# Kernel tuning notes

Hardware: AMD Instinct MI355X
Metric: run time of the kernel (lower is better)

The kernel has to match this reference:

```python
import jax, jax.numpy as jnp
import numpy as np

EPS = 1e-5

def setup_inputs() -> dict:
    key = jax.random.key(0)
    ks = jax.random.split(key, 8)
    B, C, O, H, W = 4, 256, 256, 64, 64
    x = jax.random.normal(ks[0], (B, C, H, W), jnp.float32)
    # offset/mask conv: 27 = deformable_groups(1) * 3 * kh * kw; small init so sampling points stay near grid
    w_off = jax.random.normal(ks[1], (27, C, 3, 3), jnp.float32) * 0.01
    b_off = jnp.zeros((27,), jnp.float32)
    weight = jax.random.normal(ks[2], (O, C, 3, 3), jnp.float32) * (1.0 / np.sqrt(C * 9))
    bias = jnp.zeros((O,), jnp.float32)
    gamma = 1.0 + 0.1 * jax.random.normal(ks[3], (O,), jnp.float32)
    beta = 0.1 * jax.random.normal(ks[4], (O,), jnp.float32)
    run_mean = 0.05 * jax.random.normal(ks[5], (O,), jnp.float32)
    run_var = jax.random.uniform(ks[6], (O,), jnp.float32, 0.5, 1.5)
    return {"x": x, "w_off": w_off, "b_off": b_off, "weight": weight, "bias": bias,
            "gamma": gamma, "beta": beta, "run_mean": run_mean, "run_var": run_var}

def reference(x, w_off, b_off, weight, bias, gamma, beta, run_mean, run_var):
    B, C, H, W = x.shape
    O = weight.shape[0]
    K = 9  # 3x3 kernel taps
    # conv_offset_mask: standard 3x3 conv, pad 1 -> (B, 27, H, W)
    om = jax.lax.conv_general_dilated(
        x, w_off, window_strides=(1, 1), padding=[(1, 1), (1, 1)],
        dimension_numbers=("NCHW", "OIHW", "NCHW")) + b_off[None, :, None, None]
    dy, dx = om[:, :K], om[:, K:2 * K]            # (B,9,H,W) learned offsets
    mask = jax.nn.sigmoid(om[:, 2 * K:])           # (B,9,H,W) modulation
    # base sampling grid for 3x3, stride 1, pad 1, dilation 1
    ky, kx = jnp.meshgrid(jnp.arange(3), jnp.arange(3), indexing="ij")
    ky = ky.reshape(K, 1, 1).astype(x.dtype)
    kx = kx.reshape(K, 1, 1).astype(x.dtype)
    base_y = (jnp.arange(H, dtype=x.dtype) - 1.0)[None, :, None] + ky  # (9,H,1)
    base_x = (jnp.arange(W, dtype=x.dtype) - 1.0)[None, None, :] + kx  # (9,1,W)
    py = dy + base_y  # (B,9,H,W) absolute sample coords
    px = dx + base_x
    y0 = jnp.floor(py); x0 = jnp.floor(px)
    ly = py - y0; lx = px - x0
    y0i = y0.astype(jnp.int32); x0i = x0.astype(jnp.int32)
    xf = x.reshape(B, C, H * W)

    def corner(yi, xi, wgt):
        valid = (yi >= 0) & (yi < H) & (xi >= 0) & (xi < W)  # zero-pad outside
        yc = jnp.clip(yi, 0, H - 1)
        xc = jnp.clip(xi, 0, W - 1)
        idx = (yc * W + xc).reshape(B, 1, -1)                # (B,1,9HW)
        g = jnp.take_along_axis(xf, idx, axis=2)             # (B,C,9HW)
        return g * (wgt * valid.astype(x.dtype)).reshape(B, 1, -1)

    val = (corner(y0i, x0i, (1 - ly) * (1 - lx))
           + corner(y0i, x0i + 1, (1 - ly) * lx)
           + corner(y0i + 1, x0i, ly * (1 - lx))
           + corner(y0i + 1, x0i + 1, ly * lx))
    val = val.reshape(B, C, K, H, W) * mask[:, None]          # modulated im2col
    out = jnp.einsum("bckhw,ock->bohw", val, weight.reshape(O, C, K))
    out = out + bias[None, :, None, None]
    # BN (eval mode, running stats) + ReLU
    inv = jax.lax.rsqrt(run_var + EPS)
    out = gamma[None, :, None, None] * (out - run_mean[None, :, None, None]) * inv[None, :, None, None] + beta[None, :, None, None]
    return jax.nn.relu(out)
```

## Files before the change

### kernel.cpp

```cpp
#include <hip/hip_runtime.h>
#include <math.h>

#define HW_ 4096
#define N_ 16384
#define RS2 1168
#define LDS_PK 37376
#define LDS_W4 38528
#define LDS_TOT 43136

typedef _Float16 f16x4 __attribute__((ext_vector_type(4)));
typedef _Float16 f16x8 __attribute__((ext_vector_type(8)));
typedef float f32x4 __attribute__((ext_vector_type(4)));
typedef unsigned short u16x8 __attribute__((ext_vector_type(8)));


static __device__ __forceinline__ unsigned short f2h(float f) {
  _Float16 h = (_Float16)f;
  return __builtin_bit_cast(unsigned short, h);
}
static __device__ __forceinline__ f32x4 madv(f32x4 a, float s, f32x4 c) {
  c.x = fmaf(a.x, s, c.x);
  c.y = fmaf(a.y, s, c.y);
  c.z = fmaf(a.z, s, c.z);
  c.w = fmaf(a.w, s, c.w);
  return c;
}

__global__ __launch_bounds__(256) void transp_kernel(const float* __restrict__ x,
                                                     float* __restrict__ xT) {
  __shared__ float t[64][65];
  int bid = blockIdx.x;
  int b = bid >> 8, cg = (bid >> 6) & 3, h = bid & 63;
  int tid = threadIdx.x;
  int l16 = tid & 15, r16 = tid >> 4;
  const float* xs = x + (size_t)(b * 256 + cg * 64) * HW_ + h * 64;
#pragma unroll
  for (int j = 0; j < 4; ++j) {
    int c = j * 16 + r16;
    f32x4 v = *(const f32x4*)(xs + (size_t)c * HW_ + l16 * 4);
    t[c][l16 * 4 + 0] = v.x;
    t[c][l16 * 4 + 1] = v.y;
    t[c][l16 * 4 + 2] = v.z;
    t[c][l16 * 4 + 3] = v.w;
  }
  __syncthreads();
  float* xd = xT + (size_t)(b * HW_ + h * 64) * 256 + cg * 64;
#pragma unroll
  for (int j = 0; j < 4; ++j) {
    int w2 = j * 16 + r16;
    f32x4 v;
#pragma unroll
    for (int i = 0; i < 4; ++i) v[i] = t[l16 * 4 + i][w2];
    *(f32x4*)(xd + (size_t)w2 * 256 + l16 * 4) = v;
  }
}

__global__ __launch_bounds__(256) void wprep_kernel(
    const float* __restrict__ weight, const float* __restrict__ w_off,
    const float* __restrict__ bias, const float* __restrict__ gamma,
    const float* __restrict__ beta, const float* __restrict__ rmean,
    const float* __restrict__ rvar, unsigned short* __restrict__ Wt,
    unsigned short* __restrict__ Woff, float* __restrict__ scale,
    float* __restrict__ shift) {
  int o = blockIdx.x, tid = threadIdx.x;
  __shared__ unsigned short wl[2304];
  __shared__ unsigned short wol[2304];
  const float* wrow = weight + (size_t)o * 2304;
  const float* worow = w_off + (size_t)o * 2304;
  bool do_off = (o < 32);
#pragma unroll
  for (int j = 0; j < 9; ++j) {
    int flat = tid + j * 256;
    int c = flat / 9, k = flat - 9 * c;
    int cb = c >> 6, cloc = c & 31;
    int ks = (k << 1) | ((c >> 5) & 1);
    int dst = (cb * 18 + ks) * 32 + cloc;
    wl[dst] = f2h(wrow[flat]);
    if (do_off) wol[dst] = f2h((o < 27) ? worow[flat] : 0.f);
  }
  __syncthreads();
  for (int it = tid; it < 288; it += 256) {
    int chunk = it >> 2, part = it & 3;
    *(u16x8*)&Wt[((size_t)chunk * 256 + o) * 32 + part * 8] =
        *(const u16x8*)&wl[chunk * 32 + part * 8];
    if (do_off)
      *(u16x8*)&Woff[((size_t)chunk * 32 + o) * 32 + part * 8] =
          *(const u16x8*)&wol[chunk * 32 + part * 8];
  }
  if (o == 0) {
    float inv = rsqrtf(rvar[tid] + 1e-5f);
    float sc = gamma[tid] * inv;
    scale[tid] = sc;
    shift[tid] = beta[tid] + sc * (bias[tid] - rmean[tid]);
  }
}

__global__ __launch_bounds__(512) void fused_kernel(
    const float* __restrict__ xT, const unsigned short* __restrict__ Wt,
    const unsigned short* __restrict__ Woff, const float* __restrict__ b_off,
    const float* __restrict__ scale, const float* __restrict__ shift,
    float* __restrict__ out) {
  __shared__ __align__(16) char smem[LDS_TOT];
  float* om_lds = (float*)smem;
  unsigned int* pk_lds = (unsigned int*)(smem + LDS_PK);
  float* w4_lds = (float*)(smem + LDS_W4);

  int bid = blockIdx.x;
  int swz = (bid & 7) * 64 + (bid >> 3);
  int nbase = swz * 32;
  int b = nbase >> 12;
  int h = (nbase >> 6) & 63;
  int wb = nbase & 32;

  int tid = threadIdx.x;
  int lane = tid & 63;
  int wv = tid >> 6;
  int m15 = lane & 15, q = lane >> 4;
  int sn = tid >> 4;
  int cs = tid & 15;

  const char* xb = (const char*)xT + (size_t)b * (HW_ * 256 * 4);
  char* ldr = smem + sn * RS2 + ((cs >> 3) << 6) + (cs & 7) * 8;

  int mf = (wv >> 1) & 1, nf1 = wv & 1;
  f32x4 aoff = (f32x4){0.f, 0.f, 0.f, 0.f};
  for (int cb = 0; cb < 4; ++cb) {
    {
      const char* xc = xb + cb * 256 + cs * 16;
#pragma unroll
      for (int k = 0; k < 9; ++k) {
        int ky = k / 3, kx = k - 3 * (k / 3);
        int yy = h + ky - 1, xx = wb + sn + kx - 1;
        f32x4 v = (f32x4){0.f, 0.f, 0.f, 0.f};
        if (((unsigned)yy < 64u) && ((unsigned)xx < 64u))
          v = *(const f32x4*)(xc + (size_t)(yy * 64 + xx) * 1024);
        *(f16x4*)(ldr + k * 128) = __builtin_convertvector(v, f16x4);
      }
    }
    __syncthreads();
    if (wv < 4) {
#pragma unroll
      for (int ks = 0; ks < 18; ++ks) {
        f16x8 a = *(const f16x8*)(Woff + ((cb * 18 + ks) * 32 + mf * 16 + m15) * 32 + q * 8);
        f16x8 bb = *(const f16x8*)(smem + (nf1 * 16 + m15) * RS2 + ks * 64 + q * 16);
        aoff = __builtin_amdgcn_mfma_f32_16x16x32_f16(a, bb, aoff, 0, 0, 0);
      }
    }
    __syncthreads();
  }
  if (wv < 4) {
#pragma unroll
    for (int r = 0; r < 4; ++r)
      om_lds[(mf * 16 + q * 4 + r) * 32 + nf1 * 16 + m15] = aoff[r];
  }
  __syncthreads();

  if (tid < 288) {
    int k = tid >> 5, pxl = tid & 31;
    float dy = om_lds[k * 32 + pxl] + b_off[k];
    float dx = om_lds[(k + 9) * 32 + pxl] + b_off[k + 9];
    float z = om_lds[(k + 18) * 32 + pxl] + b_off[k + 18];
    float ms = 1.f / (1.f + expf(-z));
    int ky = k / 3, kx = k - 3 * ky;
    float py = dy + (float)(h - 1 + ky);
    float pxf = dx + (float)(wb + pxl - 1 + kx);
    float fy0 = floorf(py), fx0 = floorf(pxf);
    float ly = py - fy0, lx = pxf - fx0;
    int iy0 = (int)fy0, ix0 = (int)fx0;
    bool vy0 = (iy0 >= 0) && (iy0 < 64);
    bool vy1 = (iy0 >= -1) && (iy0 < 63);
    bool vx0 = (ix0 >= 0) && (ix0 < 64);
    bool vx1 = (ix0 >= -1) && (ix0 < 63);
    int yA = min(max(iy0, 0), 63), yB = min(max(iy0 + 1, 0), 63);
    int xA = min(max(ix0, 0), 63), xB = min(max(ix0 + 1, 0), 63);
    pk_lds[k * 32 + pxl] = (unsigned)(yA * 64 + xA) | ((unsigned)(xB - xA) << 12) |
                           ((unsigned)(yB - yA) << 13);
    float* wp = w4_lds + (k * 32 + pxl) * 4;
    wp[0] = (1.f - ly) * (1.f - lx) * ms * ((vy0 && vx0) ? 1.f : 0.f);
    wp[1] = (1.f - ly) * lx * ms * ((vy0 && vx1) ? 1.f : 0.f);
    wp[2] = ly * (1.f - lx) * ms * ((vy1 && vx0) ? 1.f : 0.f);
    wp[3] = ly * lx * ms * ((vy1 && vx1) ? 1.f : 0.f);
  }
  __syncthreads();

  f32x4 acc[2][2];
#pragma unroll
  for (int mfi = 0; mfi < 2; ++mfi)
#pragma unroll
    for (int nf = 0; nf < 2; ++nf) acc[mfi][nf] = (f32x4){0.f, 0.f, 0.f, 0.f};

  f16x4 sv[9];
#define GATHER(CB)                                                     \
  {                                                                    \
    const char* xc = xb + (CB) * 256 + cs * 16;                        \
    _Pragma("unroll") for (int k = 0; k < 9; ++k) {                    \
      unsigned pv = pk_lds[k * 32 + sn];                               \
      f32x4 w4v = *(const f32x4*)(w4_lds + (k * 32 + sn) * 4);         \
      const char* p00 = xc + ((size_t)(pv & 0xFFFu) << 10);            \
      int dxb = (int)(pv & 0x1000u) >> 2;             \
      int dyb = (int)(pv & 0x2000u) << 3;             \
      f32x4 c00 = *(const f32x4*)(p00);                                \
      f32x4 c01 = *(const f32x4*)(p00 + dxb);                          \
      f32x4 c10 = *(const f32x4*)(p00 + dyb);                          \
      f32x4 c11 = *(const f32x4*)(p00 + dyb + dxb);                    \
      f32x4 v = (f32x4){0.f, 0.f, 0.f, 0.f};                           \
      v = madv(c00, w4v.x, v);                                         \
      v = madv(c01, w4v.y, v);                                         \
      v = madv(c10, w4v.z, v);                                         \
      v = madv(c11, w4v.w, v);                                         \
      sv[k] = __builtin_convertvector(v, f16x4);                       \
    }                                                                  \
  }

  GATHER(0);
  for (int cb = 0; cb < 4; ++cb) {
    {
#pragma unroll
      for (int k = 0; k < 9; ++k) *(f16x4*)(ldr + k * 128) = sv[k];
    }
    __syncthreads();
    if (cb < 3) GATHER(cb + 1);
    {
      const unsigned short* wtk = Wt + (size_t)(cb * 18) * 8192 + (wv * 32 + m15) * 32 + q * 8;
#pragma unroll
      for (int ks = 0; ks < 18; ++ks) {
        const unsigned short* wp2 = wtk + ks * 8192;
        f16x8 a0 = *(const f16x8*)(wp2);
        f16x8 a1 = *(const f16x8*)(wp2 + 512);
#pragma unroll
        for (int nf = 0; nf < 2; ++nf) {
          f16x8 bb = *(const f16x8*)(smem + (nf * 16 + m15) * RS2 + ks * 64 + q * 16);
          acc[0][nf] = __builtin_amdgcn_mfma_f32_16x16x32_f16(a0, bb, acc[0][nf], 0, 0, 0);
          acc[1][nf] = __builtin_amdgcn_mfma_f32_16x16x32_f16(a1, bb, acc[1][nf], 0, 0, 0);
        }
      }
    }
    __syncthreads();
  }

  float* ob = out + (size_t)(b * 256) * HW_ + h * 64 + wb;
#pragma unroll
  for (int mfi = 0; mfi < 2; ++mfi)
#pragma unroll
    for (int r = 0; r < 4; ++r) {
      int o = wv * 32 + mfi * 16 + q * 4 + r;
      float sc = scale[o], sh = shift[o];
#pragma unroll
      for (int nf = 0; nf < 2; ++nf) {
        float vv = fmaxf(fmaf(acc[mfi][nf][r], sc, sh), 0.f);
        ob[(size_t)o * HW_ + nf * 16 + m15] = vv;
      }
    }
}

extern "C" void kernel_launch(void* const* d_in, const int* in_sizes, int n_in,
                              void* d_out, int out_size, void* d_ws, size_t ws_size,
                              hipStream_t stream) {
  (void)in_sizes; (void)n_in; (void)out_size; (void)ws_size;
  const float* x = (const float*)d_in[0];
  const float* w_off = (const float*)d_in[1];
  const float* b_off = (const float*)d_in[2];
  const float* weight = (const float*)d_in[3];
  const float* bias = (const float*)d_in[4];
  const float* gamma = (const float*)d_in[5];
  const float* beta = (const float*)d_in[6];
  const float* rmean = (const float*)d_in[7];
  const float* rvar = (const float*)d_in[8];
  char* ws = (char*)d_ws;
  unsigned short* Wt = (unsigned short*)ws;
  unsigned short* Woff = (unsigned short*)(ws + 1179648);
  float* scale = (float*)(ws + 1327104);
  float* shift = (float*)(ws + 1328128);
  float* xT = (float*)(ws + 1329152);
  float* out = (float*)d_out;

  transp_kernel<<<dim3(1024), dim3(256), 0, stream>>>(x, xT);
  wprep_kernel<<<dim3(256), dim3(256), 0, stream>>>(weight, w_off, bias, gamma, beta,
                                                    rmean, rvar, Wt, Woff, scale, shift);
  fused_kernel<<<dim3(512), dim3(512), 0, stream>>>(xT, Wt, Woff, b_off, scale, shift, out);
}
```

Before: 184.2 us.

## Store transposed activations in fp16 and cache sampling params in registers

The transpose kernel now writes the channel-last copy of x in fp16 instead of fp32, which halves the bytes read by the offset-conv loads and the bilinear gathers in the fused kernel. The packed sample indices and bilinear weights are loaded from LDS into registers once. This lets the offset/weight LDS region overlap the staging buffer, shrinking LDS, and the kernel gets a waves_per_eu hint. Corner values are now rounded to fp16 before interpolation, which adds a small rounding error, and register pressure goes up.

```diff
diff --git a/kernel.cpp b/kernel.cpp
--- a/kernel.cpp
+++ b/kernel.cpp
@@ -4,9 +4,6 @@
 #define HW_ 4096
 #define N_ 16384
 #define RS2 1168
-#define LDS_PK 37376
-#define LDS_W4 38528
-#define LDS_TOT 43136
 
 typedef _Float16 f16x4 __attribute__((ext_vector_type(4)));
 typedef _Float16 f16x8 __attribute__((ext_vector_type(8)));
@@ -27,7 +24,7 @@
 }
 
 __global__ __launch_bounds__(256) void transp_kernel(const float* __restrict__ x,
-                                                     float* __restrict__ xT) {
+                                                     _Float16* __restrict__ xT) {
   __shared__ float t[64][65];
   int bid = blockIdx.x;
   int b = bid >> 8, cg = (bid >> 6) & 3, h = bid & 63;
@@ -44,14 +41,14 @@
     t[c][l16 * 4 + 3] = v.w;
   }
   __syncthreads();
-  float* xd = xT + (size_t)(b * HW_ + h * 64) * 256 + cg * 64;
+  _Float16* xd = xT + (size_t)(b * HW_ + h * 64) * 256 + cg * 64;
 #pragma unroll
   for (int j = 0; j < 4; ++j) {
     int w2 = j * 16 + r16;
-    f32x4 v;
-#pragma unroll
-    for (int i = 0; i < 4; ++i) v[i] = t[l16 * 4 + i][w2];
-    *(f32x4*)(xd + (size_t)w2 * 256 + l16 * 4) = v;
+    f16x4 v;
+#pragma unroll
+    for (int i = 0; i < 4; ++i) v[i] = (_Float16)t[l16 * 4 + i][w2];
+    *(f16x4*)(xd + (size_t)w2 * 256 + l16 * 4) = v;
   }
 }
 
@@ -95,15 +92,15 @@
   }
 }
 
-__global__ __launch_bounds__(512) void fused_kernel(
-    const float* __restrict__ xT, const unsigned short* __restrict__ Wt,
+__global__ __launch_bounds__(512) __attribute__((amdgpu_waves_per_eu(4, 4))) void fused_kernel(
+    const _Float16* __restrict__ xT, const unsigned short* __restrict__ Wt,
     const unsigned short* __restrict__ Woff, const float* __restrict__ b_off,
     const float* __restrict__ scale, const float* __restrict__ shift,
     float* __restrict__ out) {
-  __shared__ __align__(16) char smem[LDS_TOT];
+  __shared__ __align__(16) char smem[32 * RS2];
   float* om_lds = (float*)smem;
-  unsigned int* pk_lds = (unsigned int*)(smem + LDS_PK);
-  float* w4_lds = (float*)(smem + LDS_W4);
+  unsigned int* pk_lds = (unsigned int*)(smem + 4096);
+  float* w4_lds = (float*)(smem + 5248);
 
   int bid = blockIdx.x;
   int swz = (bid & 7) * 64 + (bid >> 3);
@@ -119,22 +116,22 @@
   int sn = tid >> 4;
   int cs = tid & 15;
 
-  const char* xb = (const char*)xT + (size_t)b * (HW_ * 256 * 4);
+  const char* xb = (const char*)xT + (size_t)b * (HW_ * 512);
   char* ldr = smem + sn * RS2 + ((cs >> 3) << 6) + (cs & 7) * 8;
 
   int mf = (wv >> 1) & 1, nf1 = wv & 1;
   f32x4 aoff = (f32x4){0.f, 0.f, 0.f, 0.f};
   for (int cb = 0; cb < 4; ++cb) {
     {
-      const char* xc = xb + cb * 256 + cs * 16;
+      const char* xc = xb + cb * 128 + cs * 8;
 #pragma unroll
       for (int k = 0; k < 9; ++k) {
         int ky = k / 3, kx = k - 3 * (k / 3);
         int yy = h + ky - 1, xx = wb + sn + kx - 1;
-        f32x4 v = (f32x4){0.f, 0.f, 0.f, 0.f};
+        f16x4 v = (f16x4){0, 0, 0, 0};
         if (((unsigned)yy < 64u) && ((unsigned)xx < 64u))
-          v = *(const f32x4*)(xc + (size_t)(yy * 64 + xx) * 1024);
-        *(f16x4*)(ldr + k * 128) = __builtin_convertvector(v, f16x4);
+          v = *(const f16x4*)(xc + (size_t)(yy * 64 + xx) * 512);
+        *(f16x4*)(ldr + k * 128) = v;
       }
     }
     __syncthreads();
@@ -183,6 +180,15 @@
   }
   __syncthreads();
 
+  unsigned int pkv[9];
+  float wf[9][4];
+#pragma unroll
+  for (int k = 0; k < 9; ++k) {
+    pkv[k] = pk_lds[k * 32 + sn];
+#pragma unroll
+    for (int j = 0; j < 4; ++j) wf[k][j] = w4_lds[(k * 32 + sn) * 4 + j];
+  }
+
   f32x4 acc[2][2];
 #pragma unroll
   for (int mfi = 0; mfi < 2; ++mfi)
@@ -190,29 +196,29 @@
     for (int nf = 0; nf < 2; ++nf) acc[mfi][nf] = (f32x4){0.f, 0.f, 0.f, 0.f};
 
   f16x4 sv[9];
-#define GATHER(CB)                                                     \
-  {                                                                    \
-    const char* xc = xb + (CB) * 256 + cs * 16;                        \
-    _Pragma("unroll") for (int k = 0; k < 9; ++k) {                    \
-      unsigned pv = pk_lds[k * 32 + sn];                               \
-      f32x4 w4v = *(const f32x4*)(w4_lds + (k * 32 + sn) * 4);         \
-      const char* p00 = xc + ((size_t)(pv & 0xFFFu) << 10);            \
-      int dxb = (int)(pv & 0x1000u) >> 2;             \
-      int dyb = (int)(pv & 0x2000u) << 3;             \
-      f32x4 c00 = *(const f32x4*)(p00);                                \
-      f32x4 c01 = *(const f32x4*)(p00 + dxb);                          \
-      f32x4 c10 = *(const f32x4*)(p00 + dyb);                          \
-      f32x4 c11 = *(const f32x4*)(p00 + dyb + dxb);                    \
-      f32x4 v = (f32x4){0.f, 0.f, 0.f, 0.f};                           \
-      v = madv(c00, w4v.x, v);                                         \
-      v = madv(c01, w4v.y, v);                                         \
-      v = madv(c10, w4v.z, v);                                         \
-      v = madv(c11, w4v.w, v);                                         \
-      sv[k] = __builtin_convertvector(v, f16x4);                       \
-    }                                                                  \
+#define GATHER(CB)                                                      \
+  {                                                                     \
+    const char* xc = xb + (CB) * 128 + cs * 8;                          \
+    _Pragma("unroll") for (int k = 0; k < 9; ++k) {                     \
+      unsigned pv = pkv[k];                                             \
+      const char* p00 = xc + ((size_t)(pv & 0xFFFu) << 9);              \
+      int dxb = (int)(pv & 0x1000u) >> 3;               \
+      int dyb = (int)(pv & 0x2000u) << 2;               \
+      f16x4 c00 = *(const f16x4*)(p00);                                 \
+      f16x4 c01 = *(const f16x4*)(p00 + dxb);                           \
+      f16x4 c10 = *(const f16x4*)(p00 + dyb);                           \
+      f16x4 c11 = *(const f16x4*)(p00 + dyb + dxb);                     \
+      f32x4 v = (f32x4){0.f, 0.f, 0.f, 0.f};                            \
+      v = madv(__builtin_convertvector(c00, f32x4), wf[k][0], v);       \
+      v = madv(__builtin_convertvector(c01, f32x4), wf[k][1], v);       \
+      v = madv(__builtin_convertvector(c10, f32x4), wf[k][2], v);       \
+      v = madv(__builtin_convertvector(c11, f32x4), wf[k][3], v);       \
+      sv[k] = __builtin_convertvector(v, f16x4);                        \
+    }                                                                   \
   }
 
   GATHER(0);
+  __syncthreads();
   for (int cb = 0; cb < 4; ++cb) {
     {
 #pragma unroll
@@ -271,7 +277,7 @@
   unsigned short* Woff = (unsigned short*)(ws + 1179648);
   float* scale = (float*)(ws + 1327104);
   float* shift = (float*)(ws + 1328128);
-  float* xT = (float*)(ws + 1329152);
+  _Float16* xT = (_Float16*)(ws + 1329152);
   float* out = (float*)d_out;
 
   transp_kernel<<<dim3(1024), dim3(256), 0, stream>>>(x, xT);
```

Result: slower. 245.7 us (+33.4%).
